# Kernel tuning notes

Measured on AMD Instinct MI355X. Metric: run time of the kernel, lower is better.

## Reference

```python
import jax, jax.numpy as jnp
import numpy as np

B, C, H, W = 8, 64, 112, 112
KEY_NUM = 9


def conv1x1(x, w, b):
    # x: [b,c,h,w], w: [co,ci], b: [co]
    return jnp.einsum('bchw,oc->bohw', x, w) + b[None, :, None, None]


def bilinear_sample(feat, dy, dx):
    # feat: [b,c,H,W]; dy,dx: [b,H,W]. Zero-padded bilinear point sampling
    # (equivalent to torchvision deform_conv2d with 1x1 identity weight).
    b, c, h, w = feat.shape
    yy = jnp.arange(h, dtype=feat.dtype)[:, None]
    xx = jnp.arange(w, dtype=feat.dtype)[None, :]
    py = dy + yy  # [b,h,w]
    px = dx + xx
    y0 = jnp.floor(py)
    x0 = jnp.floor(px)
    wy1 = py - y0
    wx1 = px - x0
    wy0 = 1.0 - wy1
    wx0 = 1.0 - wx1
    featf = feat.reshape(b, c, h * w)

    def gather(yi, xi):
        valid = (yi >= 0) & (yi < h) & (xi >= 0) & (xi < w)
        yc = jnp.clip(yi, 0, h - 1).astype(jnp.int32)
        xc = jnp.clip(xi, 0, w - 1).astype(jnp.int32)
        idx = (yc * w + xc).reshape(b, 1, h * w)
        v = jnp.take_along_axis(featf, idx, axis=2).reshape(b, c, h, w)
        return v * valid.astype(feat.dtype)[:, None]

    return (gather(y0, x0) * (wy0 * wx0)[:, None]
            + gather(y0, x0 + 1) * (wy0 * wx1)[:, None]
            + gather(y0 + 1, x0) * (wy1 * wx0)[:, None]
            + gather(y0 + 1, x0 + 1) * (wy1 * wx1)[:, None])


def setup_inputs() -> dict:
    key = jax.random.key(0)
    ks = jax.random.split(key, 8)
    s = 1.0 / np.sqrt(C)
    return {
        'query_layer': jax.random.normal(ks[0], (B, C, H, W), jnp.float32),
        'key_layer': jax.random.normal(ks[1], (B, C, H, W), jnp.float32),
        'w_refer': jax.random.normal(ks[2], (C, C), jnp.float32) * s,
        'b_refer': jax.random.normal(ks[3], (C,), jnp.float32) * 0.1,
        'w_attn': jax.random.normal(ks[4], (KEY_NUM, C), jnp.float32) * s,
        'b_attn': jax.random.normal(ks[5], (KEY_NUM,), jnp.float32) * 0.1,
        'w_off': jax.random.normal(ks[6], (2 * KEY_NUM, C), jnp.float32) * s,
        'b_off': jax.random.normal(ks[7], (2 * KEY_NUM,), jnp.float32) * 0.1,
    }


def reference(query_layer, key_layer, w_refer, b_refer, w_attn, b_attn, w_off, b_off):
    key_feature = conv1x1(key_layer, w_refer, b_refer)          # [b,c,h,w]
    attn = jax.nn.softmax(conv1x1(query_layer, w_attn, b_attn), axis=1)  # [b,K,h,w]
    offset = conv1x1(query_layer, w_off, b_off)                  # [b,2K,h,w]
    # Faithful to original: key k uses offset channels [k, k+1] (overlapping slices)
    dys = jnp.moveaxis(offset[:, 0:KEY_NUM], 1, 0)               # [K,b,h,w]
    dxs = jnp.moveaxis(offset[:, 1:KEY_NUM + 1], 1, 0)           # [K,b,h,w]
    sampled = jax.vmap(bilinear_sample, in_axes=(None, 0, 0))(key_feature, dys, dxs)  # [K,b,c,h,w]
    out = jnp.einsum('kbchw,bkhw->bchw', sampled, attn)
    return out
```

## Files before the change

kernel.cpp:

```cpp
#include <hip/hip_runtime.h>

#define BB 8
#define CC 64
#define HH 112
#define WW 112
#define HWs (HH * WW)
#define KEYN 9

#define CK_PX 128
#define CK_TILES (HWs / CK_PX)
#define CK_NBLK (BB * CK_TILES)
#define WTS 68

#define SM_PX 32
#define SM_TILES (HWs / SM_PX)
#define SM_NBLK (BB * SM_TILES)

#define OFF_WQ   0
#define OFF_SB   1280
#define OFF_L    1300
#define OFF_XQ   1972
#define OFF_P    0
#define OFF_T    0
#define OFF_OUTT 2304
#define SM_LDS   4480

__device__ __forceinline__ float swzx16(float v) {
    return __uint_as_float(__builtin_amdgcn_ds_swizzle(__float_as_uint(v), 0x401F));
}

__global__ __launch_bounds__(256, 3) void conv_key_kernel(
    const float* __restrict__ key, const float* __restrict__ w_refer,
    const float* __restrict__ b_refer, float* __restrict__ Kf)
{
    __shared__ float Xin[64 * CK_PX];
    __shared__ float Wt[64 * WTS];

    const int t = threadIdx.x;
    const int blk = blockIdx.x;
    const int b = blk / CK_TILES;
    const int s0 = (blk - b * CK_TILES) * CK_PX;
    const size_t inb = (size_t)b * CC * HWs + s0;

    #pragma unroll
    for (int m = 0; m < 4; ++m) {
        const int f = t + 256 * m;
        const int o = f >> 4;
        const int q = f & 15;
        const float4 wv = *reinterpret_cast<const float4*>(w_refer + o * CC + 4 * q);
        Wt[(4 * q + 0) * WTS + o] = wv.x;
        Wt[(4 * q + 1) * WTS + o] = wv.y;
        Wt[(4 * q + 2) * WTS + o] = wv.z;
        Wt[(4 * q + 3) * WTS + o] = wv.w;
    }
    #pragma unroll
    for (int m = 0; m < 8; ++m) {
        const int f = t + 256 * m;
        const int k = f >> 5;
        const int p8 = f & 31;
        *reinterpret_cast<float4*>(&Xin[k * CK_PX + 4 * p8]) =
            *reinterpret_cast<const float4*>(key + inb + (size_t)k * HWs + 4 * p8);
    }
    __syncthreads();

    const int og = t & 7;
    const int p4 = t >> 3;
    const float4 bias0 = *reinterpret_cast<const float4*>(b_refer + 8 * og);
    const float4 bias1 = *reinterpret_cast<const float4*>(b_refer + 8 * og + 4);
    float4 acc[4][2];
    #pragma unroll
    for (int pi = 0; pi < 4; ++pi) { acc[pi][0] = bias0; acc[pi][1] = bias1; }

    #pragma unroll 4
    for (int k = 0; k < 64; ++k) {
        const float4 a4 = *reinterpret_cast<const float4*>(&Xin[k * CK_PX + 4 * p4]);
        const float4 w0 = *reinterpret_cast<const float4*>(&Wt[k * WTS + 8 * og]);
        const float4 w1 = *reinterpret_cast<const float4*>(&Wt[k * WTS + 8 * og + 4]);
        const float ap[4] = {a4.x, a4.y, a4.z, a4.w};
        #pragma unroll
        for (int pi = 0; pi < 4; ++pi) {
            acc[pi][0].x = fmaf(ap[pi], w0.x, acc[pi][0].x);
            acc[pi][0].y = fmaf(ap[pi], w0.y, acc[pi][0].y);
            acc[pi][0].z = fmaf(ap[pi], w0.z, acc[pi][0].z);
            acc[pi][0].w = fmaf(ap[pi], w0.w, acc[pi][0].w);
            acc[pi][1].x = fmaf(ap[pi], w1.x, acc[pi][1].x);
            acc[pi][1].y = fmaf(ap[pi], w1.y, acc[pi][1].y);
            acc[pi][1].z = fmaf(ap[pi], w1.z, acc[pi][1].z);
            acc[pi][1].w = fmaf(ap[pi], w1.w, acc[pi][1].w);
        }
    }

    #pragma unroll
    for (int pi = 0; pi < 4; ++pi) {
        const size_t ob = ((size_t)b * HWs + s0 + 4 * p4 + pi) * CC + 8 * og;
        *reinterpret_cast<float4*>(Kf + ob)     = acc[pi][0];
        *reinterpret_cast<float4*>(Kf + ob + 4) = acc[pi][1];
    }
}

__device__ __forceinline__ float4 make_entry(int e, float4 pk, int s0)
{
    const int px = e & 31;
    const int c2 = (e >> 5) & 1;
    const int s = s0 + px;
    const int yi = s / WW;
    const int xi = s - yi * WW;
    const float py  = pk.y + (float)yi;
    const float pxf = pk.z + (float)xi;
    const float fy = floorf(py), fx = floorf(pxf);
    const float wy1 = py - fy, wx1 = pxf - fx;
    const int ix = (int)fx + c2;
    const int xc = min(max(ix, 0), WW - 1);
    const float vx = (ix >= 0 && ix < WW) ? 1.f : 0.f;
    const float wxc = (c2 ? wx1 : (1.f - wx1)) * vx * pk.x;
    const int iy0 = (int)fy;
    const int iy1 = iy0 + 1;
    const int yc0 = min(max(iy0, 0), HH - 1);
    const int yc1 = min(max(iy1, 0), HH - 1);
    const float w0 = ((iy0 >= 0 && iy0 < HH) ? 1.f : 0.f) * (1.f - wy1) * wxc;
    const float w1 = ((iy1 >= 0 && iy1 < HH) ? 1.f : 0.f) * wy1 * wxc;
    const unsigned a0 = (unsigned)((yc0 * WW + xc) * (CC * 4));
    const unsigned a1 = (unsigned)((yc1 * WW + xc) * (CC * 4));
    float4 r;
    r.x = __uint_as_float(a0);
    r.y = __uint_as_float(a1);
    r.z = w0;
    r.w = w1;
    return r;
}

__device__ __forceinline__ int twidx(int e)
{
    return ((e >> 6) << 6) + ((e & 31) << 1) + ((e >> 5) & 1);
}

__global__ __launch_bounds__(256, 8) void fused_sample_kernel(
    const float* __restrict__ query, const float* __restrict__ w_attn,
    const float* __restrict__ b_attn, const float* __restrict__ w_off,
    const float* __restrict__ b_off, const float* __restrict__ Kf,
    float* __restrict__ out)
{
    __shared__ float S[SM_LDS];
    float*  Wq   = S + OFF_WQ;
    float*  Sb   = S + OFF_SB;
    float*  L    = S + OFF_L;
    float*  Xq   = S + OFF_XQ;
    float4* Pf4  = reinterpret_cast<float4*>(S + OFF_P);
    float4* Tf4  = reinterpret_cast<float4*>(S + OFF_T);
    float*  OutT = S + OFF_OUTT;

    const int t = threadIdx.x;
    const int l = t & 63;
    const int w = t >> 6;
    const int blk = blockIdx.x;
    const int b = blk & 7;
    const int tile = blk >> 3;
    const int s0 = tile * SM_PX;
    const size_t qb = (size_t)b * CC * HWs + s0;
    const char* Kfb = reinterpret_cast<const char*>(Kf) + (size_t)b * HWs * CC * 4;

    for (int f = t; f < 304; f += 256) {
        const int r = f >> 4;
        const int q = f & 15;
        const float* src = (r < KEYN) ? (w_attn + r * CC) : (w_off + (r - KEYN) * CC);
        const float4 wv = *reinterpret_cast<const float4*>(src + 4 * q);
        Wq[(4 * q + 0) * 20 + r] = wv.x;
        Wq[(4 * q + 1) * 20 + r] = wv.y;
        Wq[(4 * q + 2) * 20 + r] = wv.z;
        Wq[(4 * q + 3) * 20 + r] = wv.w;
    }
    if (t < 64) Wq[t * 20 + 19] = 0.f;
    if (t < 20) Sb[t] = (t < KEYN) ? b_attn[t] : (t < 19 ? b_off[t - KEYN] : 0.f);
    #pragma unroll
    for (int m = 0; m < 2; ++m) {
        const int f = t + 256 * m;
        const int c = f >> 3;
        const int p4 = (f & 7) * 4;
        *reinterpret_cast<float4*>(&Xq[c * 32 + p4]) =
            *reinterpret_cast<const float4*>(query + qb + (size_t)c * HWs + p4);
    }
    __syncthreads();

    {
        const int px = t & 31;
        const int og = t >> 5;
        if (og < 5) {
            const int o4 = 4 * og;
            float4 acc = *reinterpret_cast<const float4*>(&Sb[o4]);
            #pragma unroll 8
            for (int k = 0; k < 64; ++k) {
                const float a = Xq[k * 32 + px];
                const float4 wv = *reinterpret_cast<const float4*>(&Wq[k * 20 + o4]);
                acc.x = fmaf(a, wv.x, acc.x);
                acc.y = fmaf(a, wv.y, acc.y);
                acc.z = fmaf(a, wv.z, acc.z);
                acc.w = fmaf(a, wv.w, acc.w);
            }
            L[px * 21 + o4 + 0] = acc.x;
            L[px * 21 + o4 + 1] = acc.y;
            L[px * 21 + o4 + 2] = acc.z;
            L[px * 21 + o4 + 3] = acc.w;
        }
    }
    __syncthreads();

    if (t < SM_PX) {
        float lg[KEYN], of[10];
        #pragma unroll
        for (int k = 0; k < KEYN; ++k) lg[k] = L[t * 21 + k];
        #pragma unroll
        for (int j = 0; j < 10; ++j) of[j] = L[t * 21 + KEYN + j];
        float m = lg[0];
        #pragma unroll
        for (int k = 1; k < KEYN; ++k) m = fmaxf(m, lg[k]);
        float s = 0.f, e[KEYN];
        #pragma unroll
        for (int k = 0; k < KEYN; ++k) { e[k] = expf(lg[k] - m); s += e[k]; }
        const float sinv = 1.0f / s;
        #pragma unroll
        for (int k = 0; k < KEYN; ++k)
            Pf4[k * 32 + t] = make_float4(e[k] * sinv, of[k], of[k + 1], 0.f);
    }
    __syncthreads();

    {
        const int px = t & 31;
        const float4 q0 = Pf4[((t      ) >> 6) * 32 + px];
        const float4 q1 = Pf4[((t + 256) >> 6) * 32 + px];
        float4 q2 = make_float4(0.f, 0.f, 0.f, 0.f);
        if (t < 64) q2 = Pf4[((t + 512) >> 6) * 32 + px];
        __syncthreads();
        Tf4[twidx(t)]       = make_entry(t,       q0, s0);
        Tf4[twidx(t + 256)] = make_entry(t + 256, q1, s0);
        if (t < 64) Tf4[twidx(t + 512)] = make_entry(t + 512, q2, s0);
    }
    __syncthreads();

    const int sub  = l >> 5;
    const int c2   = (l >> 4) & 1;
    const int cb16 = (l & 15) * 16;

    for (int j = 0; j < 4; ++j) {
        const int p = w * 8 + 2 * j + sub;
        const float4* Tp = Tf4 + p * 2 + c2;

        float4 acc0 = make_float4(0.f, 0.f, 0.f, 0.f);
        float4 acc1 = make_float4(0.f, 0.f, 0.f, 0.f);
        #pragma unroll
        for (int k = 0; k < KEYN; ++k) {
            const float4 tv = Tp[k * 64];
            const unsigned a0 = __float_as_uint(tv.x) + cb16;
            const unsigned a1 = __float_as_uint(tv.y) + cb16;
            const float4 v0 = *reinterpret_cast<const float4*>(Kfb + a0);
            const float4 v1 = *reinterpret_cast<const float4*>(Kfb + a1);
            acc0.x = fmaf(v0.x, tv.z, acc0.x); acc0.y = fmaf(v0.y, tv.z, acc0.y);
            acc0.z = fmaf(v0.z, tv.z, acc0.z); acc0.w = fmaf(v0.w, tv.z, acc0.w);
            acc1.x = fmaf(v1.x, tv.w, acc1.x); acc1.y = fmaf(v1.y, tv.w, acc1.y);
            acc1.z = fmaf(v1.z, tv.w, acc1.z); acc1.w = fmaf(v1.w, tv.w, acc1.w);
        }
        float4 acc;
        acc.x = acc0.x + acc1.x; acc.y = acc0.y + acc1.y;
        acc.z = acc0.z + acc1.z; acc.w = acc0.w + acc1.w;

        acc.x += swzx16(acc.x); acc.y += swzx16(acc.y);
        acc.z += swzx16(acc.z); acc.w += swzx16(acc.w);

        if ((l & 16) == 0) {
            float* d = OutT + p * 68 + (cb16 >> 2);
            *reinterpret_cast<float4*>(d) = acc;
        }
    }
    __syncthreads();

    const size_t ob = (size_t)b * CC * HWs + s0;
    #pragma unroll
    for (int m = 0; m < 8; ++m) {
        const int f = t + 256 * m;
        const int c = f >> 5;
        const int px = f & 31;
        out[ob + (size_t)c * HWs + px] = OutT[px * 68 + c];
    }
}

extern "C" void kernel_launch(void* const* d_in, const int* in_sizes, int n_in,
                              void* d_out, int out_size, void* d_ws, size_t ws_size,
                              hipStream_t stream)
{
    const float* query   = (const float*)d_in[0];
    const float* key     = (const float*)d_in[1];
    const float* w_refer = (const float*)d_in[2];
    const float* b_refer = (const float*)d_in[3];
    const float* w_attn  = (const float*)d_in[4];
    const float* b_attn  = (const float*)d_in[5];
    const float* w_off   = (const float*)d_in[6];
    const float* b_off   = (const float*)d_in[7];
    float* out = (float*)d_out;

    float* Kf = (float*)d_ws;

    hipLaunchKernelGGL(conv_key_kernel, dim3(CK_NBLK), dim3(256), 0, stream,
                       key, w_refer, b_refer, Kf);
    hipLaunchKernelGGL(fused_sample_kernel, dim3(SM_NBLK), dim3(256), 0, stream,
                       query, w_attn, b_attn, w_off, b_off, Kf, out);
}
```

Measured before the change: 151.9 us.

## Store key features in fp16 and restructure bilinear gather table

The intermediate key-feature tensor is now written and gathered as half precision, which halves the bytes moved by the conv store and by the random bilinear gathers. The conv kernel also drops its LDS staging of the input and reads it directly from global memory, with a higher occupancy hint and a changed block-to-batch mapping. The sampler builds one table entry per (key, pixel) holding row bases, x index and all four corner weights, and each lane gathers 8 channels, reducing with two swizzle steps. The fp16 storage reduces accuracy of the intermediate and may affect tolerance checks.

```diff
diff --git a/kernel.cpp b/kernel.cpp
--- a/kernel.cpp
+++ b/kernel.cpp
@@ -1,4 +1,5 @@
 #include <hip/hip_runtime.h>
+#include <hip/hip_fp16.h>
 
 #define BB 8
 #define CC 64
@@ -28,18 +29,20 @@
 __device__ __forceinline__ float swzx16(float v) {
     return __uint_as_float(__builtin_amdgcn_ds_swizzle(__float_as_uint(v), 0x401F));
 }
-
-__global__ __launch_bounds__(256, 3) void conv_key_kernel(
+__device__ __forceinline__ float swzx8(float v) {
+    return __uint_as_float(__builtin_amdgcn_ds_swizzle(__float_as_uint(v), 0x201F));
+}
+
+__global__ __launch_bounds__(256, 4) void conv_key_kernel(
     const float* __restrict__ key, const float* __restrict__ w_refer,
-    const float* __restrict__ b_refer, float* __restrict__ Kf)
+    const float* __restrict__ b_refer, __half* __restrict__ Kf)
 {
-    __shared__ float Xin[64 * CK_PX];
     __shared__ float Wt[64 * WTS];
 
     const int t = threadIdx.x;
     const int blk = blockIdx.x;
-    const int b = blk / CK_TILES;
-    const int s0 = (blk - b * CK_TILES) * CK_PX;
+    const int b = blk & 7;
+    const int s0 = (blk >> 3) * CK_PX;
     const size_t inb = (size_t)b * CC * HWs + s0;
 
     #pragma unroll
@@ -53,14 +56,6 @@
         Wt[(4 * q + 2) * WTS + o] = wv.z;
         Wt[(4 * q + 3) * WTS + o] = wv.w;
     }
-    #pragma unroll
-    for (int m = 0; m < 8; ++m) {
-        const int f = t + 256 * m;
-        const int k = f >> 5;
-        const int p8 = f & 31;
-        *reinterpret_cast<float4*>(&Xin[k * CK_PX + 4 * p8]) =
-            *reinterpret_cast<const float4*>(key + inb + (size_t)k * HWs + 4 * p8);
-    }
     __syncthreads();
 
     const int og = t & 7;
@@ -73,7 +68,7 @@
 
     #pragma unroll 4
     for (int k = 0; k < 64; ++k) {
-        const float4 a4 = *reinterpret_cast<const float4*>(&Xin[k * CK_PX + 4 * p4]);
+        const float4 a4 = *reinterpret_cast<const float4*>(key + inb + (size_t)k * HWs + 4 * p4);
         const float4 w0 = *reinterpret_cast<const float4*>(&Wt[k * WTS + 8 * og]);
         const float4 w1 = *reinterpret_cast<const float4*>(&Wt[k * WTS + 8 * og + 4]);
         const float ap[4] = {a4.x, a4.y, a4.z, a4.w};
@@ -93,51 +88,55 @@
     #pragma unroll
     for (int pi = 0; pi < 4; ++pi) {
         const size_t ob = ((size_t)b * HWs + s0 + 4 * p4 + pi) * CC + 8 * og;
-        *reinterpret_cast<float4*>(Kf + ob)     = acc[pi][0];
-        *reinterpret_cast<float4*>(Kf + ob + 4) = acc[pi][1];
-    }
-}
-
-__device__ __forceinline__ float4 make_entry(int e, float4 pk, int s0)
+        union { __half2 h; int i; } u0, u1, u2, u3;
+        u0.h = __floats2half2_rn(acc[pi][0].x, acc[pi][0].y);
+        u1.h = __floats2half2_rn(acc[pi][0].z, acc[pi][0].w);
+        u2.h = __floats2half2_rn(acc[pi][1].x, acc[pi][1].y);
+        u3.h = __floats2half2_rn(acc[pi][1].z, acc[pi][1].w);
+        int4 pk; pk.x = u0.i; pk.y = u1.i; pk.z = u2.i; pk.w = u3.i;
+        *reinterpret_cast<int4*>(Kf + ob) = pk;
+    }
+}
+
+struct TEnt { float4 a, b; };
+
+__device__ __forceinline__ TEnt make_entry2(int e, float4 pk, int s0)
 {
-    const int px = e & 31;
-    const int c2 = (e >> 5) & 1;
-    const int s = s0 + px;
+    const int p = e & 31;
+    const int s = s0 + p;
     const int yi = s / WW;
     const int xi = s - yi * WW;
     const float py  = pk.y + (float)yi;
     const float pxf = pk.z + (float)xi;
     const float fy = floorf(py), fx = floorf(pxf);
     const float wy1 = py - fy, wx1 = pxf - fx;
-    const int ix = (int)fx + c2;
-    const int xc = min(max(ix, 0), WW - 1);
-    const float vx = (ix >= 0 && ix < WW) ? 1.f : 0.f;
-    const float wxc = (c2 ? wx1 : (1.f - wx1)) * vx * pk.x;
-    const int iy0 = (int)fy;
-    const int iy1 = iy0 + 1;
+    const float wy0 = 1.f - wy1, wx0 = 1.f - wx1;
+    const int ix0 = (int)fx;
+    const int iy0 = (int)fy, iy1 = iy0 + 1;
+    const float vx0 = (ix0 >= 0 && ix0 < WW)      ? 1.f : 0.f;
+    const float vx1 = (ix0 >= -1 && ix0 < WW - 1) ? 1.f : 0.f;
+    const float vy0 = (iy0 >= 0 && iy0 < HH)      ? 1.f : 0.f;
+    const float vy1 = (iy1 >= 0 && iy1 < HH)      ? 1.f : 0.f;
     const int yc0 = min(max(iy0, 0), HH - 1);
     const int yc1 = min(max(iy1, 0), HH - 1);
-    const float w0 = ((iy0 >= 0 && iy0 < HH) ? 1.f : 0.f) * (1.f - wy1) * wxc;
-    const float w1 = ((iy1 >= 0 && iy1 < HH) ? 1.f : 0.f) * wy1 * wxc;
-    const unsigned a0 = (unsigned)((yc0 * WW + xc) * (CC * 4));
-    const unsigned a1 = (unsigned)((yc1 * WW + xc) * (CC * 4));
-    float4 r;
-    r.x = __uint_as_float(a0);
-    r.y = __uint_as_float(a1);
-    r.z = w0;
-    r.w = w1;
+    TEnt r;
+    r.a.x = __uint_as_float((unsigned)(yc0 * WW * 128));
+    r.a.y = __uint_as_float((unsigned)(yc1 * WW * 128));
+    r.a.z = __int_as_float(ix0);
+    r.a.w = 0.f;
+    const float ay0 = pk.x * wy0 * vy0;
+    const float ay1 = pk.x * wy1 * vy1;
+    r.b.x = ay0 * wx0 * vx0;
+    r.b.y = ay0 * wx1 * vx1;
+    r.b.z = ay1 * wx0 * vx0;
+    r.b.w = ay1 * wx1 * vx1;
     return r;
-}
-
-__device__ __forceinline__ int twidx(int e)
-{
-    return ((e >> 6) << 6) + ((e & 31) << 1) + ((e >> 5) & 1);
 }
 
 __global__ __launch_bounds__(256, 8) void fused_sample_kernel(
     const float* __restrict__ query, const float* __restrict__ w_attn,
     const float* __restrict__ b_attn, const float* __restrict__ w_off,
-    const float* __restrict__ b_off, const float* __restrict__ Kf,
+    const float* __restrict__ b_off, const __half* __restrict__ Kf,
     float* __restrict__ out)
 {
     __shared__ float S[SM_LDS];
@@ -146,7 +145,7 @@
     float*  L    = S + OFF_L;
     float*  Xq   = S + OFF_XQ;
     float4* Pf4  = reinterpret_cast<float4*>(S + OFF_P);
-    float4* Tf4  = reinterpret_cast<float4*>(S + OFF_T);
+    float*  Tb   = S + OFF_T;
     float*  OutT = S + OFF_OUTT;
 
     const int t = threadIdx.x;
@@ -157,7 +156,7 @@
     const int tile = blk >> 3;
     const int s0 = tile * SM_PX;
     const size_t qb = (size_t)b * CC * HWs + s0;
-    const char* Kfb = reinterpret_cast<const char*>(Kf) + (size_t)b * HWs * CC * 4;
+    const char* Kfb = reinterpret_cast<const char*>(Kf) + (size_t)b * HWs * 128;
 
     for (int f = t; f < 304; f += 256) {
         const int r = f >> 4;
@@ -224,50 +223,63 @@
     __syncthreads();
 
     {
-        const int px = t & 31;
-        const float4 q0 = Pf4[((t      ) >> 6) * 32 + px];
-        const float4 q1 = Pf4[((t + 256) >> 6) * 32 + px];
+        const float4 q1 = Pf4[t];
         float4 q2 = make_float4(0.f, 0.f, 0.f, 0.f);
-        if (t < 64) q2 = Pf4[((t + 512) >> 6) * 32 + px];
+        if (t < 32) q2 = Pf4[256 + t];
         __syncthreads();
-        Tf4[twidx(t)]       = make_entry(t,       q0, s0);
-        Tf4[twidx(t + 256)] = make_entry(t + 256, q1, s0);
-        if (t < 64) Tf4[twidx(t + 512)] = make_entry(t + 512, q2, s0);
-    }
-    __syncthreads();
-
-    const int sub  = l >> 5;
-    const int c2   = (l >> 4) & 1;
-    const int cb16 = (l & 15) * 16;
+        const TEnt e1 = make_entry2(t, q1, s0);
+        *reinterpret_cast<float4*>(Tb + t * 8)     = e1.a;
+        *reinterpret_cast<float4*>(Tb + t * 8 + 4) = e1.b;
+        if (t < 32) {
+            const TEnt e2 = make_entry2(256 + t, q2, s0);
+            *reinterpret_cast<float4*>(Tb + (256 + t) * 8)     = e2.a;
+            *reinterpret_cast<float4*>(Tb + (256 + t) * 8 + 4) = e2.b;
+        }
+    }
+    __syncthreads();
+
+    const int  ch8  = l & 7;
+    const bool c2b  = (l >> 3) & 1;
+    const bool rowb = (l >> 4) & 1;
+    const int  sub  = l >> 5;
+    const unsigned chb = (unsigned)(ch8 * 16);
 
     for (int j = 0; j < 4; ++j) {
         const int p = w * 8 + 2 * j + sub;
-        const float4* Tp = Tf4 + p * 2 + c2;
-
-        float4 acc0 = make_float4(0.f, 0.f, 0.f, 0.f);
-        float4 acc1 = make_float4(0.f, 0.f, 0.f, 0.f);
+        const float* Te = Tb + p * 8;
+
+        float acc[8] = {0.f, 0.f, 0.f, 0.f, 0.f, 0.f, 0.f, 0.f};
         #pragma unroll
         for (int k = 0; k < KEYN; ++k) {
-            const float4 tv = Tp[k * 64];
-            const unsigned a0 = __float_as_uint(tv.x) + cb16;
-            const unsigned a1 = __float_as_uint(tv.y) + cb16;
-            const float4 v0 = *reinterpret_cast<const float4*>(Kfb + a0);
-            const float4 v1 = *reinterpret_cast<const float4*>(Kfb + a1);
-            acc0.x = fmaf(v0.x, tv.z, acc0.x); acc0.y = fmaf(v0.y, tv.z, acc0.y);
-            acc0.z = fmaf(v0.z, tv.z, acc0.z); acc0.w = fmaf(v0.w, tv.z, acc0.w);
-            acc1.x = fmaf(v1.x, tv.w, acc1.x); acc1.y = fmaf(v1.y, tv.w, acc1.y);
-            acc1.z = fmaf(v1.z, tv.w, acc1.z); acc1.w = fmaf(v1.w, tv.w, acc1.w);
-        }
-        float4 acc;
-        acc.x = acc0.x + acc1.x; acc.y = acc0.y + acc1.y;
-        acc.z = acc0.z + acc1.z; acc.w = acc0.w + acc1.w;
-
-        acc.x += swzx16(acc.x); acc.y += swzx16(acc.y);
-        acc.z += swzx16(acc.z); acc.w += swzx16(acc.w);
-
-        if ((l & 16) == 0) {
-            float* d = OutT + p * 68 + (cb16 >> 2);
-            *reinterpret_cast<float4*>(d) = acc;
+            const float4 t1 = *reinterpret_cast<const float4*>(Te + k * 256);
+            const float4 t2 = *reinterpret_cast<const float4*>(Te + k * 256 + 4);
+            const int xi = __float_as_int(t1.z) + (c2b ? 1 : 0);
+            const int xc = min(max(xi, 0), WW - 1);
+            const unsigned rb = __float_as_uint(rowb ? t1.y : t1.x);
+            const float wgt = rowb ? (c2b ? t2.w : t2.z) : (c2b ? t2.y : t2.x);
+            const unsigned addr = rb + ((unsigned)xc << 7) + chb;
+            const int4 raw = *reinterpret_cast<const int4*>(Kfb + addr);
+            union { int i; __half2 h; } u0, u1, u2, u3;
+            u0.i = raw.x; u1.i = raw.y; u2.i = raw.z; u3.i = raw.w;
+            acc[0] = fmaf(__low2float(u0.h),  wgt, acc[0]);
+            acc[1] = fmaf(__high2float(u0.h), wgt, acc[1]);
+            acc[2] = fmaf(__low2float(u1.h),  wgt, acc[2]);
+            acc[3] = fmaf(__high2float(u1.h), wgt, acc[3]);
+            acc[4] = fmaf(__low2float(u2.h),  wgt, acc[4]);
+            acc[5] = fmaf(__high2float(u2.h), wgt, acc[5]);
+            acc[6] = fmaf(__low2float(u3.h),  wgt, acc[6]);
+            acc[7] = fmaf(__high2float(u3.h), wgt, acc[7]);
+        }
+
+        #pragma unroll
+        for (int i = 0; i < 8; ++i) acc[i] += swzx16(acc[i]);
+        #pragma unroll
+        for (int i = 0; i < 8; ++i) acc[i] += swzx8(acc[i]);
+
+        if ((l & 24) == 0) {
+            float* d = OutT + p * 68 + ch8 * 8;
+            *reinterpret_cast<float4*>(d)     = make_float4(acc[0], acc[1], acc[2], acc[3]);
+            *reinterpret_cast<float4*>(d + 4) = make_float4(acc[4], acc[5], acc[6], acc[7]);
         }
     }
     __syncthreads();
@@ -296,7 +308,7 @@
     const float* b_off   = (const float*)d_in[7];
     float* out = (float*)d_out;
 
-    float* Kf = (float*)d_ws;
+    __half* Kf = (__half*)d_ws;
 
     hipLaunchKernelGGL(conv_key_kernel, dim3(CK_NBLK), dim3(256), 0, stream,
                        key, w_refer, b_refer, Kf);
```

New measurement: 148.3 us. 1.02x faster.
